# Performance work log

Hardware: AMD Instinct MI355X
Metric: run time of the kernel (lower is better)

Reference implementation:

```python
import jax, jax.numpy as jnp
import numpy as np

H = 16          # num heads
HD = 88         # head dim = 1408 / 16
IMG = 336
PATCH = 14
THETA = 10000.0
IDX = IMG // PATCH          # 24 patches per side
SEQ = IDX * IDX + 1         # 576 patches + 1 CLS slot = 577


def _vision_rope_cos_sin():
    # Faithful to HF Llama4VisionRotaryEmbedding (rope_type='llama4', complex64):
    # 2D rope over (x, y) patch coordinates; CLS token gets zero rotation.
    img_idx = np.arange(IDX * IDX, dtype=np.int64).reshape(-1, 1)
    img_idx = np.concatenate([img_idx, img_idx[:1]], axis=0)
    img_idx[-1, -1] = -2  # CLS token marker
    fx = img_idx % IDX
    fy = img_idx // IDX
    freq_dim = HD // 2  # 44
    rope_freq = 1.0 / (THETA ** (np.arange(0, freq_dim, 2)[: freq_dim // 2].astype(np.float64) / freq_dim))
    freqs_x = np.repeat((fx + 1)[..., None] * rope_freq[None, None, :], 2, axis=-1)
    freqs_y = np.repeat((fy + 1)[..., None] * rope_freq[None, None, :], 2, axis=-1)
    freqs = np.concatenate([freqs_x, freqs_y], axis=-1)[..., ::2]  # [SEQ, 1, HD//2]
    freqs = np.where(img_idx.reshape(-1, 1, 1) < 0, 0.0, freqs)
    return jnp.asarray(np.cos(freqs), jnp.float32), jnp.asarray(np.sin(freqs), jnp.float32)


def _apply_rope(x, cos, sin):
    # x: [B, S, H, HD]; treat last dim as HD//2 complex pairs, rotate by e^{i*freq}
    xr = x.reshape(*x.shape[:-1], HD // 2, 2)
    a, b = xr[..., 0], xr[..., 1]               # [B, S, H, HD//2]
    out_r = a * cos - b * sin                   # cos/sin [S,1,HD//2] broadcast over B,H
    out_i = a * sin + b * cos
    return jnp.stack([out_r, out_i], axis=-1).reshape(x.shape)


def setup_inputs() -> dict:
    key = jax.random.key(0)
    ks = jax.random.split(key, 9)
    D = H * HD  # 1408
    B, S = 32, SEQ
    s = 0.02
    return {
        "hidden_states": jax.random.normal(ks[0], (B, S, D), jnp.float32),
        "wq": jax.random.normal(ks[1], (D, D), jnp.float32) * s,
        "bq": jax.random.normal(ks[2], (D,), jnp.float32) * s,
        "wk": jax.random.normal(ks[3], (D, D), jnp.float32) * s,
        "bk": jax.random.normal(ks[4], (D,), jnp.float32) * s,
        "wv": jax.random.normal(ks[5], (D, D), jnp.float32) * s,
        "bv": jax.random.normal(ks[6], (D,), jnp.float32) * s,
        "wo": jax.random.normal(ks[7], (D, D), jnp.float32) * s,
        "bo": jax.random.normal(ks[8], (D,), jnp.float32) * s,
    }


def reference(hidden_states, wq, bq, wk, bk, wv, bv, wo, bo):
    B, S, D = hidden_states.shape
    cos, sin = _vision_rope_cos_sin()
    # QKV projections (torch Linear convention: y = x @ W.T + b)
    q = (hidden_states @ wq.T + bq).reshape(B, S, H, HD)
    k = (hidden_states @ wk.T + bk).reshape(B, S, H, HD)
    v = (hidden_states @ wv.T + bv).reshape(B, S, H, HD)
    q = _apply_rope(q, cos, sin)
    k = _apply_rope(k, cos, sin)
    # Full (non-causal) self-attention
    scores = jnp.einsum('bqhd,bkhd->bhqk', q, k) * (HD ** -0.5)
    probs = jax.nn.softmax(scores, axis=-1)
    attn = jnp.einsum('bhqk,bkhd->bqhd', probs, v).reshape(B, S, D)
    return attn @ wo.T + bo
```

## Files before the change

### kernel.cpp

```cpp
#include <hip/hip_runtime.h>
#include <hip/hip_bf16.h>
#include <cstdint>
#include <cstddef>

#define NHEADS 16
#define HDIM   88
#define SEQLEN 577
#define NBATCH 32
#define DMODEL 1408
#define MROWS  (NBATCH * SEQLEN)
#define MTILES 145
#define MPAD   (MTILES * 128)
#define SP     592
#define DP     96
#define NFREQ  44
#define NBH    (NBATCH * NHEADS)
#define PADELEMS 6056

typedef __attribute__((ext_vector_type(8))) short short8;
typedef __attribute__((ext_vector_type(4))) short short4v;
typedef __attribute__((ext_vector_type(4))) float floatx4;

__device__ __forceinline__ unsigned short f2bf(float f) {
    union { float f; unsigned u; } v; v.f = f;
    unsigned u = v.u;
    u += 0x7fffu + ((u >> 16) & 1u);
    return (unsigned short)(u >> 16);
}

__device__ __forceinline__ void gload_lds16(const void* g, void* lds) {
    __builtin_amdgcn_global_load_lds(
        (__attribute__((address_space(1))) unsigned int*)(void*)(g ? (void*)g : (void*)g),
        (__attribute__((address_space(3))) unsigned int*)lds, 16, 0, 0);
}

__global__ void l4v_rope_table(float* __restrict__ cos_t, float* __restrict__ sin_t) {
    int idx = blockIdx.x * blockDim.x + threadIdx.x;
    if (idx >= SEQLEN * NFREQ) return;
    int s = idx / NFREQ, j = idx % NFREQ;
    float ang = 0.0f;
    if (s != SEQLEN - 1) {
        int coord = (j < 22) ? (s % 24) : (s / 24);
        int i = (j < 22) ? j : j - 22;
        float rf = __expf(-(2.0f * (float)i / 44.0f) * 9.21034037197618f);
        ang = (float)(coord + 1) * rf;
    }
    cos_t[idx] = cosf(ang);
    sin_t[idx] = sinf(ang);
}

__global__ void l4v_cvt_bf16(const float* __restrict__ in, unsigned short* __restrict__ out, int n) {
    int i = (blockIdx.x * blockDim.x + threadIdx.x) * 4;
    if (i + 3 < n) {
        float4 f = *(const float4*)(in + i);
        ushort4 o;
        o.x = f2bf(f.x); o.y = f2bf(f.y); o.z = f2bf(f.z); o.w = f2bf(f.w);
        *(ushort4*)(out + i) = o;
    } else {
        for (; i < n; i++) out[i] = f2bf(in[i]);
    }
}

__global__ void l4v_padzero(unsigned short* __restrict__ qb,
                            unsigned short* __restrict__ kb,
                            unsigned short* __restrict__ vb) {
    int idx = blockIdx.x * blockDim.x + threadIdx.x;
    if (idx >= NBH * PADELEMS) return;
    int bh = idx / PADELEMS, r = idx % PADELEMS;
    size_t off;
    if (r < 15 * 96) {
        int row = SEQLEN + r / 96, col = r % 96;
        off = ((size_t)bh * SP + row) * DP + col;
    } else {
        int rr = r - 15 * 96;
        int row = rr / 8, col = 88 + (rr % 8);
        off = ((size_t)bh * SP + row) * DP + col;
    }
    qb[off] = 0; kb[off] = 0; vb[off] = 0;
}

__global__ __launch_bounds__(256, 2)
void l4v_gemm128(const unsigned short* __restrict__ A,
                 const unsigned short* __restrict__ Bw,
                 const float* __restrict__ bias,
                 const float* __restrict__ cos_t,
                 const float* __restrict__ sin_t,
                 unsigned short* __restrict__ out_bf,
                 float* __restrict__ out_f32,
                 int mode)
{
    __shared__ __align__(16) unsigned short a_sm[128 * 32];
    __shared__ __align__(16) unsigned short b_sm[128 * 32];

    const int tid  = threadIdx.x;
    const int lane = tid & 63;
    const int w    = tid >> 6;
    const int quad = lane >> 4;
    const int c    = lane & 15;
    const int wr   = w >> 1;
    const int wc   = w & 1;
    const int m0   = blockIdx.y * 128;
    const int n0   = blockIdx.x * 128;

    floatx4 acc[4][4];
#pragma unroll
    for (int i = 0; i < 4; i++)
#pragma unroll
        for (int j = 0; j < 4; j++) acc[i][j] = (floatx4)0.0f;

    const int chunk0 = w * 128 + lane;
    const int chunk1 = w * 128 + 64 + lane;
    const int r0 = chunk0 >> 2, ch0 = chunk0 & 3;
    const int r1 = chunk1 >> 2, ch1 = chunk1 & 3;
    const unsigned short* Ab = A  + (size_t)m0 * DMODEL;
    const unsigned short* Bb = Bw + (size_t)n0 * DMODEL;

    for (int k0 = 0; k0 < DMODEL; k0 += 32) {
        gload_lds16(Ab + (size_t)r0 * DMODEL + k0 + ch0 * 8, a_sm + (w * 128) * 8);
        gload_lds16(Ab + (size_t)r1 * DMODEL + k0 + ch1 * 8, a_sm + (w * 128 + 64) * 8);
        gload_lds16(Bb + (size_t)r0 * DMODEL + k0 + ch0 * 8, b_sm + (w * 128) * 8);
        gload_lds16(Bb + (size_t)r1 * DMODEL + k0 + ch1 * 8, b_sm + (w * 128 + 64) * 8);
        __syncthreads();
        short8 af[4], bfr[4];
#pragma unroll
        for (int mt = 0; mt < 4; mt++)
            af[mt] = *(const short8*)(a_sm + (wr * 64 + mt * 16 + c) * 32 + quad * 8);
#pragma unroll
        for (int nt = 0; nt < 4; nt++)
            bfr[nt] = *(const short8*)(b_sm + (wc * 64 + nt * 16 + c) * 32 + quad * 8);
#pragma unroll
        for (int mt = 0; mt < 4; mt++)
#pragma unroll
            for (int nt = 0; nt < 4; nt++)
                acc[mt][nt] = __builtin_amdgcn_mfma_f32_16x16x32_bf16(af[mt], bfr[nt], acc[mt][nt], 0, 0, 0);
        __syncthreads();
    }

    if (mode == 3) {
#pragma unroll
        for (int mt = 0; mt < 4; mt++) {
            int mbase = m0 + wr * 64 + mt * 16 + quad * 4;
#pragma unroll
            for (int nt = 0; nt < 4; nt++) {
                int n = n0 + wc * 64 + nt * 16 + c;
                float bi = bias[n];
#pragma unroll
                for (int r = 0; r < 4; r++) {
                    int m = mbase + r;
                    if (m < MROWS) out_f32[(size_t)m * DMODEL + n] = acc[mt][nt][r] + bi;
                }
            }
        }
        return;
    }

    const bool rope = (mode < 2);
#pragma unroll
    for (int mt = 0; mt < 4; mt++) {
        int mbase = m0 + wr * 64 + mt * 16 + quad * 4;
#pragma unroll
        for (int nt = 0; nt < 4; nt++) {
            int n = n0 + wc * 64 + nt * 16 + c;
            float bi = bias[n];
            int h = n / HDIM, d = n % HDIM, j = d >> 1;
#pragma unroll
            for (int r = 0; r < 4; r++) {
                int m = mbase + r;
                int s = m % SEQLEN;
                int b = m / SEQLEN;
                float v = acc[mt][nt][r] + bi;
                float outv = v;
                if (rope) {
                    float pv = __shfl_xor(v, 1);
                    float cs = cos_t[s * NFREQ + j];
                    float sn = sin_t[s * NFREQ + j];
                    outv = ((d & 1) == 0) ? (v * cs - pv * sn) : (pv * sn + v * cs);
                }
                if (m < MROWS)
                    out_bf[((size_t)(b * NHEADS + h) * SP + s) * DP + d] = f2bf(outv);
            }
        }
    }
}

__global__ __launch_bounds__(256, 2)
void l4v_attn(const unsigned short* __restrict__ Q,
              const unsigned short* __restrict__ K,
              const unsigned short* __restrict__ V,
              unsigned short* __restrict__ Obuf)
{
    __shared__ __align__(16) unsigned short k_sm[64 * 104];
    __shared__ __align__(16) unsigned short v_sm[64 * 96];
    __shared__ __align__(16) unsigned short p_sm[4][16 * 68];

    const int tid  = threadIdx.x;
    const int lane = tid & 63;
    const int w    = tid >> 6;
    const int quad = lane >> 4;
    const int c    = lane & 15;
    const int qt   = blockIdx.x;
    const int bh   = blockIdx.y;
    const size_t base = (size_t)bh * SP * DP;

    short8 aq[3];
    {
        int qrow = qt * 64 + w * 16 + c;
        if (qrow > SP - 1) qrow = SP - 1;
#pragma unroll
        for (int ks = 0; ks < 3; ks++)
            aq[ks] = *(const short8*)(Q + base + (size_t)qrow * DP + ks * 32 + quad * 8);
    }

    float m_run[4], l_run[4];
    floatx4 o_acc[6];
#pragma unroll
    for (int r = 0; r < 4; r++) { m_run[r] = -INFINITY; l_run[r] = 0.0f; }
#pragma unroll
    for (int i = 0; i < 6; i++) o_acc[i] = (floatx4)0.0f;

    const float sl2e = 0.10660035817780522f * 1.4426950408889634f;

    for (int kt = 0; kt < 10; kt++) {
#pragma unroll
        for (int i = 0; i < 4; i++) {
            int chnk = i * 256 + tid;
            if (chnk < 64 * 13) {
                int row = chnk / 13, pos = chnk - row * 13;
                int gpos = (pos < 12) ? pos : 0;
                int krow = kt * 64 + row;
                if (krow > SP - 1) krow = SP - 1;
                gload_lds16(K + base + (size_t)krow * DP + gpos * 8, k_sm + chnk * 8);
            }
        }
#pragma unroll
        for (int i = 0; i < 3; i++) {
            int chnk = i * 256 + tid;
            int row = chnk / 12, pos = chnk - row * 12;
            int gpos = pos ^ ((row >> 3) & 3);
            int krow = kt * 64 + row;
            if (krow > SP - 1) krow = SP - 1;
            gload_lds16(V + base + (size_t)krow * DP + gpos * 8, v_sm + chnk * 8);
        }
        __syncthreads();

        floatx4 sc[4];
#pragma unroll
        for (int nt = 0; nt < 4; nt++) {
            sc[nt] = (floatx4)0.0f;
#pragma unroll
            for (int ks = 0; ks < 3; ks++) {
                short8 bk = *(const short8*)(k_sm + (nt * 16 + c) * 104 + ks * 32 + quad * 8);
                sc[nt] = __builtin_amdgcn_mfma_f32_16x16x32_bf16(aq[ks], bk, sc[nt], 0, 0, 0);
            }
        }

        float t[4][4];
#pragma unroll
        for (int nt = 0; nt < 4; nt++) {
            int skcol = kt * 64 + nt * 16 + c;
            bool valid = (skcol < SEQLEN);
#pragma unroll
            for (int r = 0; r < 4; r++)
                t[nt][r] = valid ? sc[nt][r] * sl2e : -INFINITY;
        }

        float mnew[4], alpha[4];
#pragma unroll
        for (int r = 0; r < 4; r++) {
            float v = fmaxf(fmaxf(t[0][r], t[1][r]), fmaxf(t[2][r], t[3][r]));
#pragma unroll
            for (int off = 1; off < 16; off <<= 1) v = fmaxf(v, __shfl_xor(v, off));
            mnew[r] = fmaxf(m_run[r], v);
            alpha[r] = exp2f(m_run[r] - mnew[r]);
            m_run[r] = mnew[r];
        }

        float p[4][4];
#pragma unroll
        for (int nt = 0; nt < 4; nt++)
#pragma unroll
            for (int r = 0; r < 4; r++)
                p[nt][r] = exp2f(t[nt][r] - mnew[r]);

#pragma unroll
        for (int r = 0; r < 4; r++) {
            float sm = p[0][r] + p[1][r] + p[2][r] + p[3][r];
#pragma unroll
            for (int off = 1; off < 16; off <<= 1) sm += __shfl_xor(sm, off);
            l_run[r] = l_run[r] * alpha[r] + sm;
        }

#pragma unroll
        for (int nt = 0; nt < 4; nt++)
#pragma unroll
            for (int r = 0; r < 4; r++)
                p_sm[w][(quad * 4 + r) * 68 + nt * 16 + c] = f2bf(p[nt][r]);

#pragma unroll
        for (int i = 0; i < 6; i++)
#pragma unroll
            for (int r = 0; r < 4; r++)
                o_acc[i][r] *= alpha[r];

#pragma unroll
        for (int kp = 0; kp < 2; kp++) {
            short8 ap;
            {
                short4v lo = *(const short4v*)(&p_sm[w][c * 68 + kp * 32 + quad * 8]);
                short4v hi = *(const short4v*)(&p_sm[w][c * 68 + kp * 32 + quad * 8 + 4]);
#pragma unroll
                for (int t4 = 0; t4 < 4; t4++) { ap[t4] = lo[t4]; ap[t4 + 4] = hi[t4]; }
            }
#pragma unroll
            for (int d2 = 0; d2 < 6; d2++) {
                int posx = (((d2 * 2 + (c >> 3)) ^ quad) << 3) + (c & 7);
                short8 bv;
#pragma unroll
                for (int j = 0; j < 8; j++)
                    bv[j] = (short)v_sm[(kp * 32 + quad * 8 + j) * 96 + posx];
                o_acc[d2] = __builtin_amdgcn_mfma_f32_16x16x32_bf16(ap, bv, o_acc[d2], 0, 0, 0);
            }
        }
        __syncthreads();
    }

    const int b = bh >> 4, h = bh & 15;
#pragma unroll
    for (int r = 0; r < 4; r++) {
        int sq = qt * 64 + w * 16 + quad * 4 + r;
        float il = 1.0f / l_run[r];
        if (sq < SEQLEN) {
            size_t rowoff = ((size_t)b * SEQLEN + sq) * DMODEL + h * HDIM;
#pragma unroll
            for (int d2 = 0; d2 < 6; d2++) {
                int d = d2 * 16 + c;
                if (d < HDIM) Obuf[rowoff + d] = f2bf(o_acc[d2][r] * il);
            }
        }
    }
}

extern "C" void kernel_launch(void* const* d_in, const int* in_sizes, int n_in,
                              void* d_out, int out_size, void* d_ws, size_t ws_size,
                              hipStream_t stream)
{
    const float* hs = (const float*)d_in[0];
    const float* wq = (const float*)d_in[1];
    const float* bq = (const float*)d_in[2];
    const float* wk = (const float*)d_in[3];
    const float* bk = (const float*)d_in[4];
    const float* wv = (const float*)d_in[5];
    const float* bv = (const float*)d_in[6];
    const float* wo = (const float*)d_in[7];
    const float* bo = (const float*)d_in[8];
    float* out = (float*)d_out;

    char* ws = (char*)d_ws;
    size_t off = 0;
    auto alloc = [&](size_t bytes) -> char* {
        char* p = ws + off;
        off += (bytes + 255) & ~(size_t)255;
        return p;
    };

    unsigned short* hs_bf = (unsigned short*)alloc((size_t)MPAD * DMODEL * 2);
    unsigned short* wq_bf = (unsigned short*)alloc((size_t)DMODEL * DMODEL * 2);
    unsigned short* wk_bf = (unsigned short*)alloc((size_t)DMODEL * DMODEL * 2);
    unsigned short* wv_bf = (unsigned short*)alloc((size_t)DMODEL * DMODEL * 2);
    unsigned short* wo_bf = (unsigned short*)alloc((size_t)DMODEL * DMODEL * 2);
    unsigned short* qb    = (unsigned short*)alloc((size_t)NBH * SP * DP * 2);
    unsigned short* kb    = (unsigned short*)alloc((size_t)NBH * SP * DP * 2);
    unsigned short* vbuf  = (unsigned short*)alloc((size_t)NBH * SP * DP * 2);
    float* cos_t = (float*)alloc((size_t)SEQLEN * NFREQ * 4);
    float* sin_t = (float*)alloc((size_t)SEQLEN * NFREQ * 4);
    unsigned short* attn_bf = hs_bf;

    if (off > ws_size) return;

    l4v_rope_table<<<dim3((SEQLEN * NFREQ + 255) / 256), dim3(256), 0, stream>>>(cos_t, sin_t);
    l4v_padzero<<<dim3((NBH * PADELEMS + 255) / 256), dim3(256), 0, stream>>>(qb, kb, vbuf);

    const int nhs = MROWS * DMODEL;
    l4v_cvt_bf16<<<dim3(nhs / 4 / 256), dim3(256), 0, stream>>>(hs, hs_bf, nhs);
    const int nw = DMODEL * DMODEL;
    l4v_cvt_bf16<<<dim3(nw / 4 / 256), dim3(256), 0, stream>>>(wq, wq_bf, nw);
    l4v_cvt_bf16<<<dim3(nw / 4 / 256), dim3(256), 0, stream>>>(wk, wk_bf, nw);
    l4v_cvt_bf16<<<dim3(nw / 4 / 256), dim3(256), 0, stream>>>(wv, wv_bf, nw);
    l4v_cvt_bf16<<<dim3(nw / 4 / 256), dim3(256), 0, stream>>>(wo, wo_bf, nw);

    dim3 ggrid(DMODEL / 128, MTILES);
    l4v_gemm128<<<ggrid, dim3(256), 0, stream>>>(hs_bf, wq_bf, bq, cos_t, sin_t, qb, nullptr, 0);
    l4v_gemm128<<<ggrid, dim3(256), 0, stream>>>(hs_bf, wk_bf, bk, cos_t, sin_t, kb, nullptr, 1);
    l4v_gemm128<<<ggrid, dim3(256), 0, stream>>>(hs_bf, wv_bf, bv, cos_t, sin_t, vbuf, nullptr, 2);

    l4v_attn<<<dim3(10, NBH), dim3(256), 0, stream>>>(qb, kb, vbuf, attn_bf);

    l4v_gemm128<<<ggrid, dim3(256), 0, stream>>>(attn_bf, wo_bf, bo, cos_t, sin_t, nullptr, out, 3);
}
```

Measured before the change: 1.033 ms.

## Pre-transpose V into a d-major buffer so PV MFMA operands load as vectors

Adds a small kernel that transposes each head's V from [seq][d] to [d][seq] into scratch space reusing the output buffer. The attention kernel then stages V^T tiles in LDS and reads PV B-operands with one 16-byte LDS load instead of eight scalar strided loads. The aim is to cut LDS instruction count and bank conflicts in the PV loop, at the cost of an extra kernel launch and an extra global round trip of V. Reusing the output buffer as scratch is safe only because the final GEMM overwrites it afterwards.

```diff
diff --git a/kernel.cpp b/kernel.cpp
--- a/kernel.cpp
+++ b/kernel.cpp
@@ -13,6 +13,7 @@
 #define MPAD   (MTILES * 128)
 #define SP     592
 #define DP     96
+#define SPAD   592
 #define NFREQ  44
 #define NBH    (NBATCH * NHEADS)
 #define PADELEMS 6056
@@ -79,6 +80,29 @@
     qb[off] = 0; kb[off] = 0; vb[off] = 0;
 }
 
+__global__ __launch_bounds__(256)
+void l4v_vtr(const unsigned short* __restrict__ vb, unsigned short* __restrict__ vt) {
+    __shared__ __align__(16) unsigned short t_sm[16 * 104];
+    const int tid = threadIdx.x;
+    const int bh  = blockIdx.y;
+    const int s0  = blockIdx.x * 16;
+    const size_t ibase = (size_t)bh * SP * DP;
+    const size_t obase = (size_t)bh * DP * SPAD;
+    if (tid < 192) {
+        int row = tid / 12, ch = tid % 12;
+        short8 v = *(const short8*)(vb + ibase + (size_t)(s0 + row) * DP + ch * 8);
+        *(short8*)(t_sm + row * 104 + ch * 8) = v;
+    }
+    __syncthreads();
+    if (tid < 192) {
+        int d = tid >> 1, sc = tid & 1;
+        short8 o;
+#pragma unroll
+        for (int j = 0; j < 8; j++) o[j] = (short)t_sm[(sc * 8 + j) * 104 + d];
+        *(short8*)(vt + obase + (size_t)d * SPAD + s0 + sc * 8) = o;
+    }
+}
+
 __global__ __launch_bounds__(256, 2)
 void l4v_gemm128(const unsigned short* __restrict__ A,
                  const unsigned short* __restrict__ Bw,
@@ -186,11 +210,11 @@
 __global__ __launch_bounds__(256, 2)
 void l4v_attn(const unsigned short* __restrict__ Q,
               const unsigned short* __restrict__ K,
-              const unsigned short* __restrict__ V,
+              const unsigned short* __restrict__ Vt,
               unsigned short* __restrict__ Obuf)
 {
     __shared__ __align__(16) unsigned short k_sm[64 * 104];
-    __shared__ __align__(16) unsigned short v_sm[64 * 96];
+    __shared__ __align__(16) unsigned short v_sm[96 * 72];
     __shared__ __align__(16) unsigned short p_sm[4][16 * 68];
 
     const int tid  = threadIdx.x;
@@ -201,6 +225,7 @@
     const int qt   = blockIdx.x;
     const int bh   = blockIdx.y;
     const size_t base = (size_t)bh * SP * DP;
+    const size_t vtb  = (size_t)bh * DP * SPAD;
 
     short8 aq[3];
     {
@@ -233,13 +258,14 @@
             }
         }
 #pragma unroll
-        for (int i = 0; i < 3; i++) {
+        for (int i = 0; i < 4; i++) {
             int chnk = i * 256 + tid;
-            int row = chnk / 12, pos = chnk - row * 12;
-            int gpos = pos ^ ((row >> 3) & 3);
-            int krow = kt * 64 + row;
-            if (krow > SP - 1) krow = SP - 1;
-            gload_lds16(V + base + (size_t)krow * DP + gpos * 8, v_sm + chnk * 8);
+            if (chnk < 96 * 9) {
+                int row = chnk / 9, pos = chnk - row * 9;
+                int col = kt * 64 + (pos & 7) * 8;
+                if (col > 584) col = 584;
+                gload_lds16(Vt + vtb + (size_t)row * SPAD + col, v_sm + chnk * 8);
+            }
         }
         __syncthreads();
 
@@ -313,11 +339,7 @@
             }
 #pragma unroll
             for (int d2 = 0; d2 < 6; d2++) {
-                int posx = (((d2 * 2 + (c >> 3)) ^ quad) << 3) + (c & 7);
-                short8 bv;
-#pragma unroll
-                for (int j = 0; j < 8; j++)
-                    bv[j] = (short)v_sm[(kp * 32 + quad * 8 + j) * 96 + posx];
+                short8 bv = *(const short8*)(v_sm + (d2 * 16 + c) * 72 + (kp * 4 + quad) * 8);
                 o_acc[d2] = __builtin_amdgcn_mfma_f32_16x16x32_bf16(ap, bv, o_acc[d2], 0, 0, 0);
             }
         }
@@ -374,6 +396,7 @@
     float* cos_t = (float*)alloc((size_t)SEQLEN * NFREQ * 4);
     float* sin_t = (float*)alloc((size_t)SEQLEN * NFREQ * 4);
     unsigned short* attn_bf = hs_bf;
+    unsigned short* vt = (unsigned short*)out;
 
     if (off > ws_size) return;
 
@@ -393,7 +416,9 @@
     l4v_gemm128<<<ggrid, dim3(256), 0, stream>>>(hs_bf, wk_bf, bk, cos_t, sin_t, kb, nullptr, 1);
     l4v_gemm128<<<ggrid, dim3(256), 0, stream>>>(hs_bf, wv_bf, bv, cos_t, sin_t, vbuf, nullptr, 2);
 
-    l4v_attn<<<dim3(10, NBH), dim3(256), 0, stream>>>(qb, kb, vbuf, attn_bf);
+    l4v_vtr<<<dim3(37, NBH), dim3(256), 0, stream>>>(vbuf, vt);
+
+    l4v_attn<<<dim3(10, NBH), dim3(256), 0, stream>>>(qb, kb, vt, attn_bf);
 
     l4v_gemm128<<<ggrid, dim3(256), 0, stream>>>(attn_bf, wo_bf, bo, cos_t, sin_t, nullptr, out, 3);
 }
```

New measurement: 1.014 ms. No clear change (-1.8%).
